# Kernel tuning notes

Hardware: AMD Instinct MI355X
Metric: run time of the kernel (lower is better)

## Reference

```python
import jax, jax.numpy as jnp
import numpy as np

H = 768
NH = 12
HD = H // NH
FF = 3072
EPS = 1e-12
SCALE = 1.0 / (HD ** 0.5)


def _ln(x, g, b):
    m = jnp.mean(x, axis=-1, keepdims=True)
    v = jnp.mean((x - m) ** 2, axis=-1, keepdims=True)
    return (x - m) * jax.lax.rsqrt(v + EPS) * g + b


def setup_inputs() -> dict:
    key = jax.random.key(0)
    ks = jax.random.split(key, 16)
    B, Q, S, T = 8, 64, 48, 128
    s = 0.02
    return {
        "q": jax.random.normal(ks[0], (B, Q, H), jnp.float32),
        "k": jax.random.normal(ks[1], (B, S, T, H), jnp.float32),
        "mask": jax.random.randint(ks[2], (B, S, T), 0, 2, jnp.int32),
        "Wq": jax.random.normal(ks[3], (H, H), jnp.float32) * s,
        "Wkv": jax.random.normal(ks[4], (H, H), jnp.float32) * s,
        "Wo": jax.random.normal(ks[5], (H, H), jnp.float32) * s,
        "bo": jnp.zeros((H,), jnp.float32),
        "ln1_g": jnp.ones((H,), jnp.float32),
        "ln1_b": jnp.zeros((H,), jnp.float32),
        "W1": jax.random.normal(ks[6], (H, FF), jnp.float32) * s,
        "b1": jnp.zeros((FF,), jnp.float32),
        "W2": jax.random.normal(ks[7], (FF, H), jnp.float32) * s,
        "b2": jnp.zeros((H,), jnp.float32),
        "ln2_g": jnp.ones((H,), jnp.float32),
        "ln2_b": jnp.zeros((H,), jnp.float32),
    }


def reference(q, k, mask, Wq, Wkv, Wo, bo, ln1_g, ln1_b, W1, b1, W2, b2, ln2_g, ln2_b):
    B, Q, _ = q.shape
    _, S, T, _ = k.shape
    # projections (no bias)
    qp = (q @ Wq).reshape(B, Q, NH, HD)            # [b,q,h,d]
    kv = (k @ Wkv).reshape(B, S, T, NH, HD)        # [b,s,t,h,d]
    # broadcast-query grouped attention: softmax only over token dim t
    scores = jnp.einsum('bqhd,bsthd->bhqst', qp, kv) * SCALE
    scores = scores + mask.astype(scores.dtype)[:, None, None, :, :] * -10000.0
    alpha = jax.nn.softmax(scores, axis=-1)        # dropout is identity in eval
    res = jnp.einsum('bhqst,bsthd->bqshd', alpha, kv).reshape(B, Q, S, H)
    # BertSelfOutput with zero residual (residual=False)
    attn_out = _ln(res @ Wo + bo, ln1_g, ln1_b)    # [b,q,s,H]
    # FFN
    ffn = jax.nn.gelu(attn_out @ W1 + b1, approximate=False) @ W2 + b2
    return _ln(attn_out + ffn, ln2_g, ln2_b)
```

## Files before the change

### kernel.cpp

```cpp
#include <hip/hip_runtime.h>
#include <hip/hip_bf16.h>
#include <math.h>

#define B_ 8
#define Q_ 64
#define S_ 48
#define T_ 128
#define H_ 768
#define NH_ 12
#define HD_ 64
#define FF_ 3072

typedef float f32x4 __attribute__((ext_vector_type(4)));
typedef short s16x8 __attribute__((ext_vector_type(8)));
typedef short s16x4 __attribute__((ext_vector_type(4)));

__device__ __forceinline__ float ldT(const float* p, size_t i) { return p[i]; }
__device__ __forceinline__ float ldT(const __hip_bfloat16* p, size_t i) { return __bfloat162float(p[i]); }
__device__ __forceinline__ void stT(float* p, size_t i, float v) { p[i] = v; }
__device__ __forceinline__ void stT(__hip_bfloat16* p, size_t i, float v) { p[i] = __float2bfloat16(v); }

__device__ __forceinline__ short f2bf(float f) {
  __hip_bfloat16 h = __float2bfloat16(f);
  return *reinterpret_cast<short*>(&h);
}

__device__ __forceinline__ float gelu_f(float x) {
  return 0.5f * x * (1.0f + erff(x * 0.70710678118654752f));
}

__device__ __forceinline__ void gld_lds16(const void* g, void* l) {
  __builtin_amdgcn_global_load_lds(
      (const __attribute__((address_space(1))) void*)g,
      (__attribute__((address_space(3))) void*)l, 16, 0, 0);
}

__device__ __forceinline__ int swz_off(int row, int kc) {
  return row * 64 + ((kc ^ ((row >> 1) & 3)) << 4);
}

template<typename OT, bool BIAS, bool GELU>
__global__ __launch_bounds__(256) void gemm_mfma(
    const __hip_bfloat16* __restrict__ A,
    const __hip_bfloat16* __restrict__ BT,
    const float* __restrict__ bias, OT* __restrict__ C,
    int N, int K, int nbx, int GB)
{
  __shared__ char sm[3][16384];

  const int cpx = gridDim.x >> 3;
  const int xcd = blockIdx.x & 7;
  const int ci  = blockIdx.x >> 3;
  const int gsz = GB * nbx;
  const int g   = ci / gsz;
  const int r2  = ci - g * gsz;
  const int bn  = r2 / GB;
  const int bi  = r2 - bn * GB;
  const int bm  = xcd * (cpx / nbx) + g * GB + bi;
  const int m0 = bm * 128, n0 = bn * 128;

  const int tid = threadIdx.x;
  const int lane = tid & 63;
  const int wid = tid >> 6;
  const int wr = wid >> 1, wc = wid & 1;

  const int nt = K >> 5;

  const __hip_bfloat16* pA[2];
  const __hip_bfloat16* pB[2];
  #pragma unroll
  for (int r = 0; r < 2; ++r) {
    const int c = tid + r * 256, row = c >> 2, slot = c & 3;
    const int kc = slot ^ ((row >> 1) & 3);
    pA[r] = A + (size_t)(m0 + row) * K + kc * 8;
    pB[r] = BT + (size_t)(n0 + row) * K + kc * 8;
  }
  auto stage = [&](int buf) {
    char* smA = sm[buf];
    char* smB = sm[buf] + 8192;
    #pragma unroll
    for (int r = 0; r < 2; ++r) {
      const int c16 = (tid + r * 256) * 16;
      gld_lds16(pA[r], smA + c16); pA[r] += 32;
      gld_lds16(pB[r], smB + c16); pB[r] += 32;
    }
  };

  f32x4 acc[4][4] = {};
  stage(0);
  if (nt > 1) stage(1);

  int cur = 0;
  for (int kt = 0; kt < nt; ++kt) {
    if (kt + 1 < nt) asm volatile("s_waitcnt vmcnt(4)" ::: "memory");
    else             asm volatile("s_waitcnt vmcnt(0)" ::: "memory");
    __builtin_amdgcn_s_barrier();
    asm volatile("" ::: "memory");

    const char* smA = sm[cur];
    const char* smB = sm[cur] + 8192;
    const int kc = lane >> 4, rl = lane & 15;
    s16x8 af[4], bf[4];
    #pragma unroll
    for (int m = 0; m < 4; ++m)
      af[m] = *(const s16x8*)(smA + swz_off(wr * 64 + m * 16 + rl, kc));
    #pragma unroll
    for (int n = 0; n < 4; ++n)
      bf[n] = *(const s16x8*)(smB + swz_off(wc * 64 + n * 16 + rl, kc));

    int nb = cur + 2; if (nb >= 3) nb -= 3;
    if (kt + 2 < nt) stage(nb);

    #pragma unroll
    for (int m = 0; m < 4; ++m)
      #pragma unroll
      for (int n = 0; n < 4; ++n)
        acc[m][n] = __builtin_amdgcn_mfma_f32_16x16x32_bf16(af[m], bf[n], acc[m][n], 0, 0, 0);

    ++cur; if (cur == 3) cur = 0;
  }

  const int colb = n0 + wc * 64 + (lane & 15);
  const int rowb = m0 + wr * 64 + (lane >> 4) * 4;
  float bv[4];
  #pragma unroll
  for (int n = 0; n < 4; ++n) bv[n] = BIAS ? bias[colb + n * 16] : 0.0f;
  #pragma unroll
  for (int m = 0; m < 4; ++m) {
    #pragma unroll
    for (int r = 0; r < 4; ++r) {
      const int row = rowb + m * 16 + r;
      #pragma unroll
      for (int n = 0; n < 4; ++n) {
        float v = acc[m][n][r] + bv[n];
        if (GELU) v = gelu_f(v);
        stT(C, (size_t)row * N + colb + n * 16, v);
      }
    }
  }
}

template<typename OT>
__global__ __launch_bounds__(256) void gemm64(
    const float* __restrict__ A, const float* __restrict__ W,
    OT* __restrict__ C, int M, int N, int K)
{
  __shared__ float As[16][65];
  __shared__ float Ws[16][65];
  const int tid = threadIdx.x;
  const int m0 = blockIdx.y * 64;
  const int n0 = blockIdx.x * 64;
  const int tx = (tid & 15) * 4;
  const int ty = (tid >> 4) * 4;
  float acc[4][4] = {};

  for (int k0 = 0; k0 < K; k0 += 16) {
    #pragma unroll
    for (int r = 0; r < 4; ++r) {
      int idx = tid + r * 256;
      int mm = idx >> 4, kk = idx & 15;
      As[kk][mm] = A[(size_t)(m0 + mm) * K + (k0 + kk)];
    }
    #pragma unroll
    for (int r = 0; r < 4; ++r) {
      int idx = tid + r * 256;
      int kk = idx >> 6, nn = idx & 63;
      Ws[kk][nn] = W[(size_t)(k0 + kk) * N + (n0 + nn)];
    }
    __syncthreads();
    #pragma unroll
    for (int kk = 0; kk < 16; ++kk) {
      float a[4], b[4];
      #pragma unroll
      for (int i = 0; i < 4; ++i) a[i] = As[kk][ty + i];
      #pragma unroll
      for (int j = 0; j < 4; ++j) b[j] = Ws[kk][tx + j];
      #pragma unroll
      for (int i = 0; i < 4; ++i)
        #pragma unroll
        for (int j = 0; j < 4; ++j) acc[i][j] += a[i] * b[j];
    }
    __syncthreads();
  }
  #pragma unroll
  for (int i = 0; i < 4; ++i)
    #pragma unroll
    for (int j = 0; j < 4; ++j)
      stT(C, (size_t)(m0 + ty + i) * N + (n0 + tx + j), acc[i][j]);
}

__global__ __launch_bounds__(256) void transpose_cast(
    const float* __restrict__ W, __hip_bfloat16* __restrict__ WT, int K, int N)
{
  __shared__ float t[32][33];
  const int n0 = blockIdx.x * 32, k0 = blockIdx.y * 32;
  const int x = threadIdx.x & 31, y4 = (threadIdx.x >> 5) * 4;
  #pragma unroll
  for (int i = 0; i < 4; ++i)
    t[y4 + i][x] = W[(size_t)(k0 + y4 + i) * N + n0 + x];
  __syncthreads();
  #pragma unroll
  for (int i = 0; i < 4; ++i)
    WT[(size_t)(n0 + y4 + i) * K + k0 + x] = __float2bfloat16(t[x][y4 + i]);
}

__global__ __launch_bounds__(256) void cast_f32_bf16(
    const float* __restrict__ x, __hip_bfloat16* __restrict__ y, size_t n4)
{
  const size_t i = (size_t)blockIdx.x * 256 + threadIdx.x;
  if (i >= n4) return;
  const float4 v = ((const float4*)x)[i];
  __hip_bfloat16 o[4] = { __float2bfloat16(v.x), __float2bfloat16(v.y),
                          __float2bfloat16(v.z), __float2bfloat16(v.w) };
  *(ushort4*)(y + i * 4) = *(ushort4*)o;
}

__global__ __launch_bounds__(256) void attn_mfma(
    const __hip_bfloat16* __restrict__ qp,
    const __hip_bfloat16* __restrict__ kvp,
    const int* __restrict__ mask,
    __hip_bfloat16* __restrict__ res)
{
  const int s = blockIdx.x, h = blockIdx.y, b = blockIdx.z;
  __shared__ __align__(16) char lds[66048];
  char* Ks = lds;
  char* VT = lds + 16384;
  char* SC = lds + 32768;
  float* mv = (float*)(lds + 65536);

  const int tid = threadIdx.x;
  const int lane = tid & 63;
  const int wid = tid >> 6;
  const int wr = wid >> 1, wc = wid & 1;
  const int kcg = lane >> 4, rl = lane & 15;

  if (tid < 128) mv[tid] = (float)mask[((size_t)b * S_ + s) * T_ + tid] * -10000.0f;

  {
    const __hip_bfloat16* qb = qp + ((size_t)b * Q_) * H_ + h * HD_;
    #pragma unroll
    for (int r = 0; r < 2; ++r) {
      const int c = tid + r * 256;
      const int qq = c >> 3, sc = c & 7;
      const int kc8 = sc ^ (qq & 7);
      gld_lds16(qb + (size_t)qq * H_ + kc8 * 8, SC + c * 16);
    }
  }
  {
    const int kc8 = tid & 7, tg = tid >> 3;
    const int t0 = tg * 4;
    const __hip_bfloat16* kb = kvp + (((size_t)b * S_ + s) * T_) * H_ + h * HD_ + kc8 * 8;
    s16x8 r0 = *(const s16x8*)(kb + (size_t)(t0 + 0) * H_);
    s16x8 r1 = *(const s16x8*)(kb + (size_t)(t0 + 1) * H_);
    s16x8 r2 = *(const s16x8*)(kb + (size_t)(t0 + 2) * H_);
    s16x8 r3 = *(const s16x8*)(kb + (size_t)(t0 + 3) * H_);
    *(s16x8*)(Ks + (t0 + 0) * 128 + ((kc8 ^ ((t0 + 0) & 7)) << 4)) = r0;
    *(s16x8*)(Ks + (t0 + 1) * 128 + ((kc8 ^ ((t0 + 1) & 7)) << 4)) = r1;
    *(s16x8*)(Ks + (t0 + 2) * 128 + ((kc8 ^ ((t0 + 2) & 7)) << 4)) = r2;
    *(s16x8*)(Ks + (t0 + 3) * 128 + ((kc8 ^ ((t0 + 3) & 7)) << 4)) = r3;
    const int tc = tg >> 1;
    const int toff = (tg & 1) * 8;
    #pragma unroll
    for (int j = 0; j < 8; ++j) {
      s16x4 v4 = { r0[j], r1[j], r2[j], r3[j] };
      const int d = kc8 * 8 + j;
      *(s16x4*)(VT + d * 256 + ((tc ^ (d & 15)) << 4) + toff) = v4;
    }
  }
  __syncthreads();

  f32x4 acc[2][4] = {};
  {
    s16x8 af[2][2], bf[2][4];
    #pragma unroll
    for (int kk = 0; kk < 2; ++kk) {
      #pragma unroll
      for (int m = 0; m < 2; ++m) {
        const int q = wr * 32 + m * 16 + rl;
        const int kc8 = kk * 4 + kcg;
        af[kk][m] = *(const s16x8*)(SC + q * 128 + ((kc8 ^ (q & 7)) << 4));
      }
      #pragma unroll
      for (int n = 0; n < 4; ++n) {
        const int t = wc * 64 + n * 16 + rl;
        const int kc8 = kk * 4 + kcg;
        bf[kk][n] = *(const s16x8*)(Ks + t * 128 + ((kc8 ^ (t & 7)) << 4));
      }
    }
    #pragma unroll
    for (int kk = 0; kk < 2; ++kk)
      #pragma unroll
      for (int m = 0; m < 2; ++m)
        #pragma unroll
        for (int n = 0; n < 4; ++n)
          acc[m][n] = __builtin_amdgcn_mfma_f32_16x16x32_bf16(af[kk][m], bf[kk][n], acc[m][n], 0, 0, 0);
  }
  __syncthreads();

  #pragma unroll
  for (int m = 0; m < 2; ++m)
    #pragma unroll
    for (int n = 0; n < 4; ++n)
      #pragma unroll
      for (int r = 0; r < 4; ++r) {
        const int q = wr * 32 + m * 16 + (lane >> 4) * 4 + r;
        const int t = wc * 64 + n * 16 + rl;
        const int tc32 = t >> 2;
        *(float*)(SC + q * 512 + ((tc32 ^ (q & 31)) << 4) + (t & 3) * 4) =
            acc[m][n][r] * 0.125f + mv[t];
      }
  __syncthreads();

  {
    const int q = tid >> 2, quarter = tid & 3;
    float vals[32];
    #pragma unroll
    for (int j = 0; j < 8; ++j) {
      const int tc32 = quarter * 8 + j;
      const f32x4 c = *(const f32x4*)(SC + q * 512 + ((tc32 ^ (q & 31)) << 4));
      vals[j * 4 + 0] = c[0]; vals[j * 4 + 1] = c[1];
      vals[j * 4 + 2] = c[2]; vals[j * 4 + 3] = c[3];
    }
    float mx = -1e30f;
    #pragma unroll
    for (int i = 0; i < 32; ++i) mx = fmaxf(mx, vals[i]);
    mx = fmaxf(mx, __shfl_xor(mx, 1, 64));
    mx = fmaxf(mx, __shfl_xor(mx, 2, 64));
    float sum = 0.0f;
    #pragma unroll
    for (int i = 0; i < 32; ++i) { vals[i] = expf(vals[i] - mx); sum += vals[i]; }
    sum += __shfl_xor(sum, 1, 64);
    sum += __shfl_xor(sum, 2, 64);
    const float inv = 1.0f / sum;
    #pragma unroll
    for (int jj = 0; jj < 4; ++jj) {
      const int tcp = quarter * 4 + jj;
      s16x8 pk;
      #pragma unroll
      for (int i = 0; i < 8; ++i) pk[i] = f2bf(vals[jj * 8 + i] * inv);
      *(s16x8*)(SC + q * 512 + ((tcp ^ (q & 15)) << 4)) = pk;
    }
  }
  __syncthreads();

  f32x4 oacc[2][2] = {};
  #pragma unroll
  for (int kt = 0; kt < 4; ++kt) {
    s16x8 pa[2], vb[2];
    #pragma unroll
    for (int m = 0; m < 2; ++m) {
      const int q = wr * 32 + m * 16 + rl;
      const int tcp = kt * 4 + kcg;
      pa[m] = *(const s16x8*)(SC + q * 512 + ((tcp ^ (q & 15)) << 4));
    }
    #pragma unroll
    for (int n = 0; n < 2; ++n) {
      const int d = wc * 32 + n * 16 + rl;
      const int tc = kt * 4 + kcg;
      vb[n] = *(const s16x8*)(VT + d * 256 + ((tc ^ (d & 15)) << 4));
    }
    #pragma unroll
    for (int m = 0; m < 2; ++m)
      #pragma unroll
      for (int n = 0; n < 2; ++n)
        oacc[m][n] = __builtin_amdgcn_mfma_f32_16x16x32_bf16(pa[m], vb[n], oacc[m][n], 0, 0, 0);
  }
  #pragma unroll
  for (int m = 0; m < 2; ++m)
    #pragma unroll
    for (int n = 0; n < 2; ++n)
      #pragma unroll
      for (int r = 0; r < 4; ++r) {
        const int q = wr * 32 + m * 16 + (lane >> 4) * 4 + r;
        const int d = wc * 32 + n * 16 + rl;
        res[(((size_t)b * Q_ + q) * S_ + s) * H_ + h * HD_ + d] =
            __float2bfloat16(oacc[m][n][r]);
      }
}

template<bool ADD, typename IT, typename OT>
__global__ __launch_bounds__(256) void ln_kernel(
    const IT* __restrict__ X, const IT* __restrict__ X2,
    const float* __restrict__ g, const float* __restrict__ bta,
    OT* __restrict__ Y)
{
  const size_t row = blockIdx.x;
  const int tid = threadIdx.x;
  float v[3];
  #pragma unroll
  for (int i = 0; i < 3; ++i) {
    int c = tid + i * 256;
    v[i] = ldT(X, row * H_ + c);
    if (ADD) v[i] += ldT(X2, row * H_ + c);
  }
  float sum = v[0] + v[1] + v[2];
  #pragma unroll
  for (int off = 32; off > 0; off >>= 1) sum += __shfl_down(sum, off, 64);
  __shared__ float red[8];
  const int w = tid >> 6;
  if ((tid & 63) == 0) red[w] = sum;
  __syncthreads();
  const float mean = (red[0] + red[1] + red[2] + red[3]) * (1.0f / 768.0f);
  float vs = 0.0f;
  #pragma unroll
  for (int i = 0; i < 3; ++i) { v[i] -= mean; vs += v[i] * v[i]; }
  #pragma unroll
  for (int off = 32; off > 0; off >>= 1) vs += __shfl_down(vs, off, 64);
  if ((tid & 63) == 0) red[4 + w] = vs;
  __syncthreads();
  const float rstd = rsqrtf((red[4] + red[5] + red[6] + red[7]) * (1.0f / 768.0f) + 1e-12f);
  #pragma unroll
  for (int i = 0; i < 3; ++i) {
    int c = tid + i * 256;
    stT(Y, row * H_ + c, v[i] * rstd * g[c] + bta[c]);
  }
}

extern "C" void kernel_launch(void* const* d_in, const int* in_sizes, int n_in,
                              void* d_out, int out_size, void* d_ws, size_t ws_size,
                              hipStream_t stream) {
  const float* q    = (const float*)d_in[0];
  const float* k    = (const float*)d_in[1];
  const int*   mask = (const int*)d_in[2];
  const float* Wq   = (const float*)d_in[3];
  const float* Wkv  = (const float*)d_in[4];
  const float* Wo   = (const float*)d_in[5];
  const float* bo   = (const float*)d_in[6];
  const float* ln1g = (const float*)d_in[7];
  const float* ln1b = (const float*)d_in[8];
  const float* W1   = (const float*)d_in[9];
  const float* b1   = (const float*)d_in[10];
  const float* W2   = (const float*)d_in[11];
  const float* b2   = (const float*)d_in[12];
  const float* ln2g = (const float*)d_in[13];
  const float* ln2b = (const float*)d_in[14];
  float* out = (float*)d_out;

  const int MROWS = B_ * Q_ * S_;
  const int KVROWS = B_ * S_ * T_;

  char* ws = (char*)d_ws;
  __hip_bfloat16* kbf  = (__hip_bfloat16*)ws;
  __hip_bfloat16* apre = (__hip_bfloat16*)ws;
  __hip_bfloat16* kvp  = (__hip_bfloat16*)(ws + 75497472);
  __hip_bfloat16* ffn1 = (__hip_bfloat16*)ws;
  __hip_bfloat16* ares = (__hip_bfloat16*)(ws + 150994944);
  __hip_bfloat16* ffn2 = ares;
  __hip_bfloat16* aln  = (__hip_bfloat16*)(ws + 188743680);
  __hip_bfloat16* qp   = (__hip_bfloat16*)(ws + 226492416);
  __hip_bfloat16* WkvT = (__hip_bfloat16*)(ws + 228065280);
  __hip_bfloat16* WoT  = (__hip_bfloat16*)(ws + 229244928);
  __hip_bfloat16* W1T  = (__hip_bfloat16*)(ws + 230424576);
  __hip_bfloat16* W2T  = (__hip_bfloat16*)(ws + 235143168);

  dim3 blk(256);

  transpose_cast<<<dim3(24, 24), blk, 0, stream>>>(Wkv, WkvT, H_, H_);
  transpose_cast<<<dim3(24, 24), blk, 0, stream>>>(Wo, WoT, H_, H_);
  transpose_cast<<<dim3(96, 24), blk, 0, stream>>>(W1, W1T, H_, FF_);
  transpose_cast<<<dim3(24, 96), blk, 0, stream>>>(W2, W2T, FF_, H_);
  cast_f32_bf16<<<dim3((KVROWS * H_ / 4 + 255) / 256), blk, 0, stream>>>(
      k, kbf, (size_t)KVROWS * H_ / 4);

  gemm64<__hip_bfloat16><<<dim3(H_ / 64, 512 / 64), blk, 0, stream>>>(
      q, Wq, qp, 512, H_, H_);
  gemm_mfma<__hip_bfloat16, false, false>
      <<<dim3((KVROWS / 128) * (H_ / 128)), blk, 0, stream>>>(
      kbf, WkvT, nullptr, kvp, H_, H_, H_ / 128, 6);
  attn_mfma<<<dim3(S_, NH_, B_), blk, 0, stream>>>(qp, kvp, mask, ares);
  gemm_mfma<__hip_bfloat16, true, false>
      <<<dim3((MROWS / 128) * (H_ / 128)), blk, 0, stream>>>(
      ares, WoT, bo, apre, H_, H_, H_ / 128, 6);
  ln_kernel<false, __hip_bfloat16, __hip_bfloat16><<<MROWS, blk, 0, stream>>>(
      apre, nullptr, ln1g, ln1b, aln);
  gemm_mfma<__hip_bfloat16, true, true>
      <<<dim3((MROWS / 128) * (FF_ / 128)), blk, 0, stream>>>(
      aln, W1T, b1, ffn1, FF_, H_, FF_ / 128, 6);
  gemm_mfma<__hip_bfloat16, true, false>
      <<<dim3((MROWS / 128) * (H_ / 128)), blk, 0, stream>>>(
      ffn1, W2T, b2, ffn2, H_, FF_, H_ / 128, 4);
  ln_kernel<true, __hip_bfloat16, float><<<MROWS, blk, 0, stream>>>(
      aln, ffn2, ln2g, ln2b, out);
}
```

Measured before the change: 629.6 us.

## Enlarge MFMA GEMM block tile to 256x128 with 128x64 per-wave tiles

The bf16 MFMA GEMM now computes a 256-row by 128-column tile per block: each of the four waves owns 128x64 outputs held in 8x4 accumulators, and A staging doubles to four 16-byte loads per thread per k-step. Swizzled LDS offsets for the A and B fragments are computed once before the main loop instead of on every iteration. The goal is more MFMA work per LDS fragment load and less global traffic per output, at the cost of more registers, 72 KB of LDS per block and half as many blocks in each GEMM launch. The wait count is raised to match the extra outstanding loads.

```diff
diff --git a/kernel.cpp b/kernel.cpp
--- a/kernel.cpp
+++ b/kernel.cpp
@@ -35,10 +35,6 @@
       (__attribute__((address_space(3))) void*)l, 16, 0, 0);
 }
 
-__device__ __forceinline__ int swz_off(int row, int kc) {
-  return row * 64 + ((kc ^ ((row >> 1) & 3)) << 4);
-}
-
 template<typename OT, bool BIAS, bool GELU>
 __global__ __launch_bounds__(256) void gemm_mfma(
     const __hip_bfloat16* __restrict__ A,
@@ -46,7 +42,7 @@
     const float* __restrict__ bias, OT* __restrict__ C,
     int N, int K, int nbx, int GB)
 {
-  __shared__ char sm[3][16384];
+  __shared__ char sm[3][24576];
 
   const int cpx = gridDim.x >> 3;
   const int xcd = blockIdx.x & 7;
@@ -57,62 +53,81 @@
   const int bn  = r2 / GB;
   const int bi  = r2 - bn * GB;
   const int bm  = xcd * (cpx / nbx) + g * GB + bi;
-  const int m0 = bm * 128, n0 = bn * 128;
+  const int m0 = bm * 256, n0 = bn * 128;
 
   const int tid = threadIdx.x;
   const int lane = tid & 63;
   const int wid = tid >> 6;
-  const int wr = wid >> 1, wc = wid & 1;
+  const int wm = wid >> 1;
+  const int wc = wid & 1;
+  const int kcg = lane >> 4, rl = lane & 15;
 
   const int nt = K >> 5;
 
-  const __hip_bfloat16* pA[2];
+  const __hip_bfloat16* pA[4];
   const __hip_bfloat16* pB[2];
+  #pragma unroll
+  for (int r = 0; r < 4; ++r) {
+    const int c = tid + r * 256, row = c >> 2, slot = c & 3;
+    const int kc = slot ^ ((row >> 1) & 3);
+    pA[r] = A + (size_t)(m0 + row) * K + kc * 8;
+  }
   #pragma unroll
   for (int r = 0; r < 2; ++r) {
     const int c = tid + r * 256, row = c >> 2, slot = c & 3;
     const int kc = slot ^ ((row >> 1) & 3);
-    pA[r] = A + (size_t)(m0 + row) * K + kc * 8;
     pB[r] = BT + (size_t)(n0 + row) * K + kc * 8;
   }
   auto stage = [&](int buf) {
     char* smA = sm[buf];
-    char* smB = sm[buf] + 8192;
+    char* smB = sm[buf] + 16384;
+    #pragma unroll
+    for (int r = 0; r < 4; ++r) {
+      gld_lds16(pA[r], smA + (tid + r * 256) * 16); pA[r] += 32;
+    }
     #pragma unroll
     for (int r = 0; r < 2; ++r) {
-      const int c16 = (tid + r * 256) * 16;
-      gld_lds16(pA[r], smA + c16); pA[r] += 32;
-      gld_lds16(pB[r], smB + c16); pB[r] += 32;
+      gld_lds16(pB[r], smB + (tid + r * 256) * 16); pB[r] += 32;
     }
   };
 
-  f32x4 acc[4][4] = {};
+  int woffA[8], woffB[4];
+  #pragma unroll
+  for (int m = 0; m < 8; ++m) {
+    const int row = wm * 128 + m * 16 + rl;
+    woffA[m] = row * 64 + ((kcg ^ ((row >> 1) & 3)) << 4);
+  }
+  #pragma unroll
+  for (int n = 0; n < 4; ++n) {
+    const int row = wc * 64 + n * 16 + rl;
+    woffB[n] = 16384 + row * 64 + ((kcg ^ ((row >> 1) & 3)) << 4);
+  }
+
+  f32x4 acc[8][4] = {};
   stage(0);
   if (nt > 1) stage(1);
 
   int cur = 0;
   for (int kt = 0; kt < nt; ++kt) {
-    if (kt + 1 < nt) asm volatile("s_waitcnt vmcnt(4)" ::: "memory");
+    if (kt + 1 < nt) asm volatile("s_waitcnt vmcnt(6)" ::: "memory");
     else             asm volatile("s_waitcnt vmcnt(0)" ::: "memory");
     __builtin_amdgcn_s_barrier();
     asm volatile("" ::: "memory");
 
-    const char* smA = sm[cur];
-    const char* smB = sm[cur] + 8192;
-    const int kc = lane >> 4, rl = lane & 15;
-    s16x8 af[4], bf[4];
-    #pragma unroll
-    for (int m = 0; m < 4; ++m)
-      af[m] = *(const s16x8*)(smA + swz_off(wr * 64 + m * 16 + rl, kc));
+    const char* bufp = sm[cur];
+    s16x8 af[8], bf[4];
+    #pragma unroll
+    for (int m = 0; m < 8; ++m)
+      af[m] = *(const s16x8*)(bufp + woffA[m]);
     #pragma unroll
     for (int n = 0; n < 4; ++n)
-      bf[n] = *(const s16x8*)(smB + swz_off(wc * 64 + n * 16 + rl, kc));
+      bf[n] = *(const s16x8*)(bufp + woffB[n]);
 
     int nb = cur + 2; if (nb >= 3) nb -= 3;
     if (kt + 2 < nt) stage(nb);
 
     #pragma unroll
-    for (int m = 0; m < 4; ++m)
+    for (int m = 0; m < 8; ++m)
       #pragma unroll
       for (int n = 0; n < 4; ++n)
         acc[m][n] = __builtin_amdgcn_mfma_f32_16x16x32_bf16(af[m], bf[n], acc[m][n], 0, 0, 0);
@@ -120,13 +135,13 @@
     ++cur; if (cur == 3) cur = 0;
   }
 
-  const int colb = n0 + wc * 64 + (lane & 15);
-  const int rowb = m0 + wr * 64 + (lane >> 4) * 4;
+  const int colb = n0 + wc * 64 + rl;
+  const int rowb = m0 + wm * 128 + (lane >> 4) * 4;
   float bv[4];
   #pragma unroll
   for (int n = 0; n < 4; ++n) bv[n] = BIAS ? bias[colb + n * 16] : 0.0f;
   #pragma unroll
-  for (int m = 0; m < 4; ++m) {
+  for (int m = 0; m < 8; ++m) {
     #pragma unroll
     for (int r = 0; r < 4; ++r) {
       const int row = rowb + m * 16 + r;
@@ -465,19 +480,19 @@
   gemm64<__hip_bfloat16><<<dim3(H_ / 64, 512 / 64), blk, 0, stream>>>(
       q, Wq, qp, 512, H_, H_);
   gemm_mfma<__hip_bfloat16, false, false>
-      <<<dim3((KVROWS / 128) * (H_ / 128)), blk, 0, stream>>>(
+      <<<dim3((KVROWS / 256) * (H_ / 128)), blk, 0, stream>>>(
       kbf, WkvT, nullptr, kvp, H_, H_, H_ / 128, 6);
   attn_mfma<<<dim3(S_, NH_, B_), blk, 0, stream>>>(qp, kvp, mask, ares);
   gemm_mfma<__hip_bfloat16, true, false>
-      <<<dim3((MROWS / 128) * (H_ / 128)), blk, 0, stream>>>(
+      <<<dim3((MROWS / 256) * (H_ / 128)), blk, 0, stream>>>(
       ares, WoT, bo, apre, H_, H_, H_ / 128, 6);
   ln_kernel<false, __hip_bfloat16, __hip_bfloat16><<<MROWS, blk, 0, stream>>>(
       apre, nullptr, ln1g, ln1b, aln);
   gemm_mfma<__hip_bfloat16, true, true>
-      <<<dim3((MROWS / 128) * (FF_ / 128)), blk, 0, stream>>>(
+      <<<dim3((MROWS / 256) * (FF_ / 128)), blk, 0, stream>>>(
       aln, W1T, b1, ffn1, FF_, H_, FF_ / 128, 6);
   gemm_mfma<__hip_bfloat16, true, false>
-      <<<dim3((MROWS / 128) * (H_ / 128)), blk, 0, stream>>>(
+      <<<dim3((MROWS / 256) * (H_ / 128)), blk, 0, stream>>>(
       ffn1, W2T, b2, ffn2, H_, FF_, H_ / 128, 4);
   ln_kernel<true, __hip_bfloat16, float><<<MROWS, blk, 0, stream>>>(
       aln, ffn2, ln2g, ln2b, out);
```

New measurement: 823.8 us. +30.8%, slower.

## Use wider 128x192 MFMA tiles for FFN GEMMs and faster tanh-style GELU

Applied to the files above, without the earlier changes.

Adds a gemm_fat kernel with 128x192 tiles (4x6 MFMA accumulators per wave), launch bounds for two blocks per CU, and triple-buffered LDS staging, and uses it for both FFN GEMMs. The larger tile raises arithmetic intensity and reuse of A loads, at the cost of more registers. The GELU epilogue swaps erff for an exp-based tanh-form approximation, which is cheaper but deviates slightly from exact GELU.

```diff
diff --git a/kernel.cpp b/kernel.cpp
--- a/kernel.cpp
+++ b/kernel.cpp
@@ -26,7 +26,10 @@
 }
 
 __device__ __forceinline__ float gelu_f(float x) {
-  return 0.5f * x * (1.0f + erff(x * 0.70710678118654752f));
+  float z = 1.5957691216f * (x + 0.044715f * x * x * x);
+  z = fminf(z, 80.0f);
+  float e = __expf(z);
+  return x * e / (e + 1.0f);
 }
 
 __device__ __forceinline__ void gld_lds16(const void* g, void* l) {
@@ -132,6 +135,122 @@
       const int row = rowb + m * 16 + r;
       #pragma unroll
       for (int n = 0; n < 4; ++n) {
+        float v = acc[m][n][r] + bv[n];
+        if (GELU) v = gelu_f(v);
+        stT(C, (size_t)row * N + colb + n * 16, v);
+      }
+    }
+  }
+}
+
+template<typename OT, bool BIAS, bool GELU>
+__global__ __launch_bounds__(256, 2) void gemm_fat(
+    const __hip_bfloat16* __restrict__ A,
+    const __hip_bfloat16* __restrict__ BT,
+    const float* __restrict__ bias, OT* __restrict__ C,
+    int N, int K, int nbx, int GB)
+{
+  __shared__ char sm[3][20480];
+
+  const int cpx = gridDim.x >> 3;
+  const int xcd = blockIdx.x & 7;
+  const int ci  = blockIdx.x >> 3;
+  const int gsz = GB * nbx;
+  const int g   = ci / gsz;
+  const int r2  = ci - g * gsz;
+  const int bn  = r2 / GB;
+  const int bi  = r2 - bn * GB;
+  const int bm  = xcd * (cpx / nbx) + g * GB + bi;
+  const int m0 = bm * 128, n0 = bn * 192;
+
+  const int tid = threadIdx.x;
+  const int lane = tid & 63;
+  const int wid = tid >> 6;
+  const int wm = wid >> 1;
+  const int wn = wid & 1;
+  const int kcg = lane >> 4, rl = lane & 15;
+
+  const int nt = K >> 5;
+
+  const __hip_bfloat16* pA[2];
+  const __hip_bfloat16* pB[3];
+  #pragma unroll
+  for (int r = 0; r < 2; ++r) {
+    const int c = tid + r * 256, row = c >> 2, slot = c & 3;
+    const int kc = slot ^ ((row >> 1) & 3);
+    pA[r] = A + (size_t)(m0 + row) * K + kc * 8;
+  }
+  #pragma unroll
+  for (int r = 0; r < 3; ++r) {
+    const int c = tid + r * 256, row = c >> 2, slot = c & 3;
+    const int kc = slot ^ ((row >> 1) & 3);
+    pB[r] = BT + (size_t)(n0 + row) * K + kc * 8;
+  }
+  auto stage = [&](int buf) {
+    char* smA = sm[buf];
+    char* smB = sm[buf] + 8192;
+    #pragma unroll
+    for (int r = 0; r < 2; ++r) {
+      gld_lds16(pA[r], smA + (tid + r * 256) * 16); pA[r] += 32;
+    }
+    #pragma unroll
+    for (int r = 0; r < 3; ++r) {
+      gld_lds16(pB[r], smB + (tid + r * 256) * 16); pB[r] += 32;
+    }
+  };
+
+  int woffA[4], woffB[6];
+  #pragma unroll
+  for (int m = 0; m < 4; ++m)
+    woffA[m] = swz_off(wm * 64 + m * 16 + rl, kcg);
+  #pragma unroll
+  for (int n = 0; n < 6; ++n)
+    woffB[n] = 8192 + swz_off(wn * 96 + n * 16 + rl, kcg);
+
+  f32x4 acc[4][6] = {};
+  stage(0);
+  if (nt > 1) stage(1);
+
+  int cur = 0;
+  for (int kt = 0; kt < nt; ++kt) {
+    if (kt + 1 < nt) asm volatile("s_waitcnt vmcnt(5)" ::: "memory");
+    else             asm volatile("s_waitcnt vmcnt(0)" ::: "memory");
+    __builtin_amdgcn_s_barrier();
+    asm volatile("" ::: "memory");
+
+    const char* bufp = sm[cur];
+    s16x8 af[4], bf[6];
+    #pragma unroll
+    for (int m = 0; m < 4; ++m)
+      af[m] = *(const s16x8*)(bufp + woffA[m]);
+    #pragma unroll
+    for (int n = 0; n < 6; ++n)
+      bf[n] = *(const s16x8*)(bufp + woffB[n]);
+
+    int nb = cur + 2; if (nb >= 3) nb -= 3;
+    if (kt + 2 < nt) stage(nb);
+
+    #pragma unroll
+    for (int m = 0; m < 4; ++m)
+      #pragma unroll
+      for (int n = 0; n < 6; ++n)
+        acc[m][n] = __builtin_amdgcn_mfma_f32_16x16x32_bf16(af[m], bf[n], acc[m][n], 0, 0, 0);
+
+    ++cur; if (cur == 3) cur = 0;
+  }
+
+  const int colb = n0 + wn * 96 + rl;
+  const int rowb = m0 + wm * 64 + (lane >> 4) * 4;
+  float bv[6];
+  #pragma unroll
+  for (int n = 0; n < 6; ++n) bv[n] = BIAS ? bias[colb + n * 16] : 0.0f;
+  #pragma unroll
+  for (int m = 0; m < 4; ++m) {
+    #pragma unroll
+    for (int r = 0; r < 4; ++r) {
+      const int row = rowb + m * 16 + r;
+      #pragma unroll
+      for (int n = 0; n < 6; ++n) {
         float v = acc[m][n][r] + bv[n];
         if (GELU) v = gelu_f(v);
         stT(C, (size_t)row * N + colb + n * 16, v);
@@ -473,12 +592,12 @@
       ares, WoT, bo, apre, H_, H_, H_ / 128, 6);
   ln_kernel<false, __hip_bfloat16, __hip_bfloat16><<<MROWS, blk, 0, stream>>>(
       apre, nullptr, ln1g, ln1b, aln);
-  gemm_mfma<__hip_bfloat16, true, true>
-      <<<dim3((MROWS / 128) * (FF_ / 128)), blk, 0, stream>>>(
-      aln, W1T, b1, ffn1, FF_, H_, FF_ / 128, 6);
-  gemm_mfma<__hip_bfloat16, true, false>
-      <<<dim3((MROWS / 128) * (H_ / 128)), blk, 0, stream>>>(
-      ffn1, W2T, b2, ffn2, H_, FF_, H_ / 128, 4);
+  gemm_fat<__hip_bfloat16, true, true>
+      <<<dim3((MROWS / 128) * (FF_ / 192)), blk, 0, stream>>>(
+      aln, W1T, b1, ffn1, FF_, H_, FF_ / 192, 6);
+  gemm_fat<__hip_bfloat16, true, false>
+      <<<dim3((MROWS / 128) * (H_ / 192)), blk, 0, stream>>>(
+      ffn1, W2T, b2, ffn2, H_, FF_, H_ / 192, 6);
   ln_kernel<true, __hip_bfloat16, float><<<MROWS, blk, 0, stream>>>(
       aln, ffn2, ln2g, ln2b, out);
 }
```

Result: faster. 605.9 us (-3.8%).
